# Performance work log

Hardware: AMD Instinct MI355X
Metric: run time of the kernel (lower is better)

Reference implementation:

```python
import jax, jax.numpy as jnp
import numpy as np


def _bilinear_gather(img, y, x):
    """Bilinear sample img [B,C,H,W] at float coords y,x [B,K,H,W] with zero padding.
    Returns [B,C,K,H,W]."""
    B, C, H, W = img.shape
    K = y.shape[1]
    y0 = jnp.floor(y)
    x0 = jnp.floor(x)
    wy = y - y0  # fractional weights [B,K,H,W]
    wx = x - x0
    y0i = y0.astype(jnp.int32)
    x0i = x0.astype(jnp.int32)
    flat = img.reshape(B, C, 1, H * W)

    def gather(yi, xi):
        valid = (yi >= 0) & (yi < H) & (xi >= 0) & (xi < W)  # [B,K,H,W]
        idx = jnp.clip(yi, 0, H - 1) * W + jnp.clip(xi, 0, W - 1)
        v = jnp.take_along_axis(flat, idx.reshape(B, 1, K, H * W), axis=-1)
        v = v.reshape(B, C, K, H, W)
        return v * valid[:, None].astype(img.dtype)

    v00 = gather(y0i, x0i)
    v01 = gather(y0i, x0i + 1)
    v10 = gather(y0i + 1, x0i)
    v11 = gather(y0i + 1, x0i + 1)
    wy_ = wy[:, None]  # [B,1,K,H,W]
    wx_ = wx[:, None]
    return (v00 * (1 - wy_) * (1 - wx_) + v01 * (1 - wy_) * wx_
            + v10 * wy_ * (1 - wx_) + v11 * wy_ * wx_)


def deform_conv2d(inp, offsets, ker):
    """torchvision.ops.deform_conv2d with stride=1, dilation=1, padding=k//2, groups=1."""
    B, C, H, W = inp.shape
    Co, Ci, k, _ = ker.shape
    pad = k // 2
    K = k * k
    off = offsets.reshape(B, K, 2, H, W)
    dy = off[:, :, 0]  # [B,K,H,W] (y offset first per torchvision convention)
    dx = off[:, :, 1]
    ii, jj = jnp.meshgrid(jnp.arange(k), jnp.arange(k), indexing='ij')
    ky = ii.reshape(K).astype(inp.dtype)  # kernel tap row index
    kx = jj.reshape(K).astype(inp.dtype)
    hgrid = jnp.arange(H, dtype=inp.dtype)
    wgrid = jnp.arange(W, dtype=inp.dtype)
    # sampling coords: p = out_pos - pad + tap + offset
    y = dy + (hgrid[None, None, :, None] - pad) + ky[None, :, None, None]
    x = dx + (wgrid[None, None, None, :] - pad) + kx[None, :, None, None]
    sampled = _bilinear_gather(inp, y, x)  # [B,C,K,H,W]
    return jnp.einsum('bckhw,ock->bohw', sampled, ker.reshape(Co, Ci, K))


def setup_inputs() -> dict:
    key = jax.random.key(0)
    k1, k2, k3, k4 = jax.random.split(key, 4)
    B, C, H, W, Co, k = 4, 16, 256, 256, 16, 3
    offsets = jax.random.normal(k1, (B, 2 * k * k, H, W), dtype=jnp.float32)
    inp = jax.random.normal(k2, (B, C, H, W), dtype=jnp.float32)
    ker = jax.random.normal(k3, (Co, C, k, k), dtype=jnp.float32) * 0.1
    target = jax.random.normal(k4, (B, Co, H, W), dtype=jnp.float32)
    return {"offsets": offsets, "input": inp, "ker": ker, "target": target}


def reference(offsets, input, ker, target):
    deformed = deform_conv2d(input, offsets, ker)
    # criterion = MSELoss (mean reduction)
    loss = jnp.mean((deformed - target) ** 2)
    return loss
```

## Files before the change

### kernel.cpp

```cpp
#include <hip/hip_runtime.h>

#define B_  4
#define C_  16
#define H_  256
#define W_  256
#define CO_ 16
#define KS_ 3
#define KK_ 9
#define HW_ (H_ * W_)
#define IMG_WORDS ((size_t)B_ * HW_ * 8)
#define KER_OFF   IMG_WORDS
#define NKB 5
#define NBLK 2048
#define PART_OFF (KER_OFF + (size_t)NKB * 256)

typedef __attribute__((ext_vector_type(8))) short bf16x8;
typedef __attribute__((ext_vector_type(4))) float f32x4;
union U4S8 { uint4 u; bf16x8 s; };

#define LOBF(u) __uint_as_float((u) << 16)
#define HIBF(u) __uint_as_float((u) & 0xffff0000u)

__device__ __forceinline__ unsigned rne_bf16(float v) {
    unsigned b = __float_as_uint(v);
    return (b + 0x7fffu + ((b >> 16) & 1u)) >> 16;
}

__global__ __launch_bounds__(256) void pack_nhwc_bf16(
    const float* __restrict__ inp, const float* __restrict__ ker,
    unsigned* __restrict__ wsu)
{
    const int t = threadIdx.x;
    const int e = blockIdx.x * 256 + t;
    const int b = e >> 16;
    const int hw = e & (HW_ - 1);
    const float* src = inp + (size_t)b * (C_ * HW_) + hw;
    float v[C_];
#pragma unroll
    for (int c = 0; c < C_; c++)
        v[c] = src[c * HW_];
    unsigned u[8];
#pragma unroll
    for (int j = 0; j < 8; j++)
        u[j] = rne_bf16(v[2 * j]) | (rne_bf16(v[2 * j + 1]) << 16);
    uint4* dst = ((uint4*)wsu) + (size_t)e * 2;
    dst[0] = make_uint4(u[0], u[1], u[2], u[3]);
    dst[1] = make_uint4(u[4], u[5], u[6], u[7]);

    if (blockIdx.x == 0) {
        for (int i = t; i < NKB * 256; i += 256) {
            const int wj  = i & 3;
            const int l   = (i >> 2) & 63;
            const int blk = i >> 8;
            const int o   = l & 15;
            unsigned lo = 0, hi = 0;
            {
                int j = 2 * wj, k = (l >> 4) * 8 + j;
                int tap = 2 * blk + (k >> 4), c = k & 15;
                if (tap <= 8) lo = rne_bf16(ker[(o * C_ + c) * KK_ + tap]);
                j = 2 * wj + 1; k = (l >> 4) * 8 + j;
                tap = 2 * blk + (k >> 4); c = k & 15;
                if (tap <= 8) hi = rne_bf16(ker[(o * C_ + c) * KK_ + tap]);
            }
            wsu[KER_OFF + i] = lo | (hi << 16);
        }
    }
}

__device__ __forceinline__ void tap_setup(
    int h, int w, int kk, float dy, float dx,
    int* idx, float* wt)
{
    const float y = dy + (float)(h - 1 + kk / KS_);
    const float x = dx + (float)(w - 1 + kk % KS_);
    const float y0f = floorf(y);
    const float x0f = floorf(x);
    const int   y0  = (int)y0f;
    const int   x0  = (int)x0f;
    const float wy  = y - y0f;
    const float wx  = x - x0f;

    float w00 = (1.f - wy) * (1.f - wx);
    float w01 = (1.f - wy) * wx;
    float w10 = wy * (1.f - wx);
    float w11 = wy * wx;

    const bool v0y = ((unsigned)y0       < (unsigned)H_);
    const bool v1y = ((unsigned)(y0 + 1) < (unsigned)H_);
    const bool v0x = ((unsigned)x0       < (unsigned)W_);
    const bool v1x = ((unsigned)(x0 + 1) < (unsigned)W_);

    wt[0] = (v0y & v0x) ? w00 : 0.f;
    wt[1] = (v0y & v1x) ? w01 : 0.f;
    wt[2] = (v1y & v0x) ? w10 : 0.f;
    wt[3] = (v1y & v1x) ? w11 : 0.f;

    const int y0c = min(max(y0,     0), H_ - 1);
    const int y1c = min(max(y0 + 1, 0), H_ - 1);
    const int x0c = min(max(x0,     0), W_ - 1);
    const int x1c = min(max(x0 + 1, 0), W_ - 1);

    idx[0] = y0c * W_ + x0c;
    idx[1] = y0c * W_ + x1c;
    idx[2] = y1c * W_ + x0c;
    idx[3] = y1c * W_ + x1c;
}

__device__ __forceinline__ unsigned blendpack(
    unsigned a, unsigned b, unsigned c, unsigned d,
    float w0, float w1, float w2, float w3)
{
    const float lo = w0 * LOBF(a) + w1 * LOBF(b) + w2 * LOBF(c) + w3 * LOBF(d);
    const float hi = w0 * HIBF(a) + w1 * HIBF(b) + w2 * HIBF(c) + w3 * HIBF(d);
    return __builtin_amdgcn_perm(__float_as_uint(hi), __float_as_uint(lo),
                                 0x07060302u);
}

__global__ __launch_bounds__(256) void deform_loss_mfma(
    const float* __restrict__ off, const unsigned* __restrict__ wsu,
    const float* __restrict__ tgt, float* __restrict__ partials)
{
    const int f = (blockIdx.x & 7) * 256 + (blockIdx.x >> 3);
    const int t = threadIdx.x;
    const int l = t & 63;
    const int q = l >> 4;
    const int m = l & 15;
    const int base = f * 128 + (t >> 6) * 32;
    const int b    = base >> 16;
    const int hwb  = base & (HW_ - 1);
    const int h    = hwb >> 8;
    const int w0   = (hwb & (W_ - 1)) + m;

    const float* offp = off + (size_t)b * (2 * KK_ * HW_) + (size_t)h * W_;
    const uint4* ib   = ((const uint4*)wsu) + (size_t)b * HW_ * 2;
    const uint4* kb   = (const uint4*)(wsu + KER_OFF);

    bf16x8 bfr[NKB];
#pragma unroll
    for (int kbk = 0; kbk < NKB; kbk++) {
        U4S8 cv; cv.u = kb[kbk * 64 + l];
        bfr[kbk] = cv.s;
    }

    float dyv[2][NKB], dxv[2][NKB];
#pragma unroll
    for (int g = 0; g < 2; g++)
#pragma unroll
        for (int kbk = 0; kbk < NKB; kbk++) {
            const int tap = min(2 * kbk + (q >> 1), KK_ - 1);
            dyv[g][kbk] = offp[(size_t)(2 * tap) * HW_ + w0 + 16 * g];
            dxv[g][kbk] = offp[(size_t)(2 * tap + 1) * HW_ + w0 + 16 * g];
        }
    const float* tbase = tgt + (size_t)b * (CO_ * HW_) + (size_t)m * HW_
                       + hwb + 4 * q;
    const float4 tv0 = *(const float4*)(tbase);
    const float4 tv1 = *(const float4*)(tbase + 16);

    f32x4 acc[2] = {{0.f, 0.f, 0.f, 0.f}, {0.f, 0.f, 0.f, 0.f}};
    uint4 cor[2][4];
    float wts[2][4];

    {
        int idx[4];
        tap_setup(h, w0, min(q >> 1, KK_ - 1), dyv[0][0], dxv[0][0], idx, wts[0]);
#pragma unroll
        for (int i = 0; i < 4; i++) cor[0][i] = ib[idx[i] * 2 + (q & 1)];
    }

#pragma unroll
    for (int kbi = 0; kbi < 2 * NKB; kbi++) {
        const int cur = kbi & 1, nxt = cur ^ 1;
        if (kbi + 1 < 2 * NKB) {
            const int gn = (kbi + 1) / NKB, kn = (kbi + 1) % NKB;
            int idx[4];
            tap_setup(h, w0 + 16 * gn, min(2 * kn + (q >> 1), KK_ - 1),
                      dyv[gn][kn], dxv[gn][kn], idx, wts[nxt]);
#pragma unroll
            for (int i = 0; i < 4; i++) cor[nxt][i] = ib[idx[i] * 2 + (q & 1)];
        }

        const int g = kbi / NKB, kkb = kbi % NKB;
        const float w0_ = wts[cur][0], w1_ = wts[cur][1],
                    w2_ = wts[cur][2], w3_ = wts[cur][3];
        const uint4 c0 = cor[cur][0], c1 = cor[cur][1],
                    c2 = cor[cur][2], c3 = cor[cur][3];
        uint4 A4;
        A4.x = blendpack(c0.x, c1.x, c2.x, c3.x, w0_, w1_, w2_, w3_);
        A4.y = blendpack(c0.y, c1.y, c2.y, c3.y, w0_, w1_, w2_, w3_);
        A4.z = blendpack(c0.z, c1.z, c2.z, c3.z, w0_, w1_, w2_, w3_);
        A4.w = blendpack(c0.w, c1.w, c2.w, c3.w, w0_, w1_, w2_, w3_);
        U4S8 ca; ca.u = A4;

        acc[g] = __builtin_amdgcn_mfma_f32_16x16x32_bf16(ca.s, bfr[kkb],
                                                         acc[g], 0, 0, 0);
    }

    float d0 = acc[0][0] - tv0.x, d1 = acc[0][1] - tv0.y,
          d2 = acc[0][2] - tv0.z, d3 = acc[0][3] - tv0.w;
    float e0 = acc[1][0] - tv1.x, e1 = acc[1][1] - tv1.y,
          e2 = acc[1][2] - tv1.z, e3 = acc[1][3] - tv1.w;
    float part = (d0 * d0 + d1 * d1 + d2 * d2 + d3 * d3
                + e0 * e0 + e1 * e1 + e2 * e2 + e3 * e3)
               * (1.0f / (float)((size_t)B_ * CO_ * HW_));

#pragma unroll
    for (int sft = 32; sft > 0; sft >>= 1)
        part += __shfl_down(part, sft, 64);

    __shared__ float red[4];
    if (l == 0)
        red[t >> 6] = part;
    __syncthreads();
    if (t == 0)
        partials[blockIdx.x] = red[0] + red[1] + red[2] + red[3];
}

__global__ __launch_bounds__(256) void reduce_partials(
    const float* __restrict__ partials, float* __restrict__ out)
{
    const int t = threadIdx.x;
    float s = 0.f;
#pragma unroll
    for (int i = 0; i < NBLK / 256; i++)
        s += partials[t + i * 256];
#pragma unroll
    for (int sft = 32; sft > 0; sft >>= 1)
        s += __shfl_down(s, sft, 64);
    __shared__ float red[4];
    if ((t & 63) == 0) red[t >> 6] = s;
    __syncthreads();
    if (t == 0) out[0] = red[0] + red[1] + red[2] + red[3];
}

__global__ __launch_bounds__(256) void deform_loss_kernel(
    const float* __restrict__ off, const float* __restrict__ inp,
    const float* __restrict__ ker, const float* __restrict__ tgt,
    float* __restrict__ out)
{
    const int idx = blockIdx.x * blockDim.x + threadIdx.x;
    float part = 0.f;
    if (idx < B_ * H_ * W_) {
        const int w  = idx & (W_ - 1);
        const int h  = (idx >> 8) & (H_ - 1);
        const int b  = idx >> 16;
        const int hw = h * W_ + w;
        const float* offb = off + (size_t)b * (2 * KK_ * HW_);
        const float* inpb = inp + (size_t)b * (C_ * HW_);
        float acc[CO_];
#pragma unroll
        for (int o = 0; o < CO_; o++) acc[o] = 0.f;
        for (int kk = 0; kk < KK_; kk++) {
            const float dy = offb[(2 * kk)     * HW_ + hw];
            const float dx = offb[(2 * kk + 1) * HW_ + hw];
            const float y = dy + (float)(h - 1 + kk / KS_);
            const float x = dx + (float)(w - 1 + kk % KS_);
            const float y0f = floorf(y);
            const float x0f = floorf(x);
            const int   y0  = (int)y0f;
            const int   x0  = (int)x0f;
            const float wy  = y - y0f;
            const float wx  = x - x0f;
            float w00 = (1.f - wy) * (1.f - wx);
            float w01 = (1.f - wy) * wx;
            float w10 = wy * (1.f - wx);
            float w11 = wy * wx;
            const bool v0y = ((unsigned)y0       < (unsigned)H_);
            const bool v1y = ((unsigned)(y0 + 1) < (unsigned)H_);
            const bool v0x = ((unsigned)x0       < (unsigned)W_);
            const bool v1x = ((unsigned)(x0 + 1) < (unsigned)W_);
            w00 = (v0y & v0x) ? w00 : 0.f;
            w01 = (v0y & v1x) ? w01 : 0.f;
            w10 = (v1y & v0x) ? w10 : 0.f;
            w11 = (v1y & v1x) ? w11 : 0.f;
            const int i00 = min(max(y0,0),H_-1)*W_ + min(max(x0,0),W_-1);
            const int i01 = min(max(y0,0),H_-1)*W_ + min(max(x0+1,0),W_-1);
            const int i10 = min(max(y0+1,0),H_-1)*W_ + min(max(x0,0),W_-1);
            const int i11 = min(max(y0+1,0),H_-1)*W_ + min(max(x0+1,0),W_-1);
            for (int c = 0; c < C_; c++) {
                const float* pp = inpb + c * HW_;
                const float s = pp[i00]*w00 + pp[i01]*w01 + pp[i10]*w10 + pp[i11]*w11;
#pragma unroll
                for (int o = 0; o < CO_; o++)
                    acc[o] = fmaf(s, ker[(o * C_ + c) * KK_ + kk], acc[o]);
            }
        }
        const float* tb = tgt + (size_t)b * (CO_ * HW_);
#pragma unroll
        for (int o = 0; o < CO_; o++) {
            const float d = acc[o] - tb[o * HW_ + hw];
            part = fmaf(d, d, part);
        }
        part *= (1.0f / (float)((size_t)B_ * CO_ * HW_));
    }
#pragma unroll
    for (int sft = 32; sft > 0; sft >>= 1)
        part += __shfl_down(part, sft, 64);
    if ((threadIdx.x & 63) == 0)
        atomicAdd(out, part);
}

extern "C" void kernel_launch(void* const* d_in, const int* in_sizes, int n_in,
                              void* d_out, int out_size, void* d_ws, size_t ws_size,
                              hipStream_t stream) {
    const float* offsets = (const float*)d_in[0];
    const float* input   = (const float*)d_in[1];
    const float* ker     = (const float*)d_in[2];
    const float* target  = (const float*)d_in[3];
    float* out = (float*)d_out;

    const size_t need = (PART_OFF + NBLK) * sizeof(unsigned);
    if (ws_size >= need) {
        unsigned* wsu = (unsigned*)d_ws;
        pack_nhwc_bf16<<<(B_ * HW_) / 256, 256, 0, stream>>>(input, ker, wsu);
        deform_loss_mfma<<<NBLK, 256, 0, stream>>>(
            offsets, wsu, target, (float*)(wsu + PART_OFF));
        reduce_partials<<<1, 256, 0, stream>>>(
            (const float*)(wsu + PART_OFF), out);
    } else {
        hipMemsetAsync(out, 0, sizeof(float), stream);
        const int total = B_ * H_ * W_;
        deform_loss_kernel<<<(total + 255) / 256, 256, 0, stream>>>(
            offsets, input, ker, target, out);
    }
}
```

Before: 114.3 us.

## Drop reduce kernel via atomics, vectorize blend, skip padded tap gathers

```diff
diff --git a/kernel.cpp b/kernel.cpp
--- a/kernel.cpp
+++ b/kernel.cpp
@@ -12,10 +12,10 @@
 #define KER_OFF   IMG_WORDS
 #define NKB 5
 #define NBLK 2048
-#define PART_OFF (KER_OFF + (size_t)NKB * 256)
 
 typedef __attribute__((ext_vector_type(8))) short bf16x8;
 typedef __attribute__((ext_vector_type(4))) float f32x4;
+typedef __attribute__((ext_vector_type(2))) float f32x2;
 union U4S8 { uint4 u; bf16x8 s; };
 
 #define LOBF(u) __uint_as_float((u) << 16)
@@ -28,7 +28,7 @@
 
 __global__ __launch_bounds__(256) void pack_nhwc_bf16(
     const float* __restrict__ inp, const float* __restrict__ ker,
-    unsigned* __restrict__ wsu)
+    unsigned* __restrict__ wsu, float* __restrict__ out)
 {
     const int t = threadIdx.x;
     const int e = blockIdx.x * 256 + t;
@@ -48,6 +48,7 @@
     dst[1] = make_uint4(u[4], u[5], u[6], u[7]);
 
     if (blockIdx.x == 0) {
+        if (t == 0) out[0] = 0.f;
         for (int i = t; i < NKB * 256; i += 256) {
             const int wj  = i & 3;
             const int l   = (i >> 2) & 63;
@@ -110,15 +111,21 @@
     unsigned a, unsigned b, unsigned c, unsigned d,
     float w0, float w1, float w2, float w3)
 {
-    const float lo = w0 * LOBF(a) + w1 * LOBF(b) + w2 * LOBF(c) + w3 * LOBF(d);
-    const float hi = w0 * HIBF(a) + w1 * HIBF(b) + w2 * HIBF(c) + w3 * HIBF(d);
-    return __builtin_amdgcn_perm(__float_as_uint(hi), __float_as_uint(lo),
+    f32x2 va = {LOBF(a), HIBF(a)};
+    f32x2 vb = {LOBF(b), HIBF(b)};
+    f32x2 vc = {LOBF(c), HIBF(c)};
+    f32x2 vd = {LOBF(d), HIBF(d)};
+    f32x2 r = va * w0;
+    r += vb * w1;
+    r += vc * w2;
+    r += vd * w3;
+    return __builtin_amdgcn_perm(__float_as_uint(r.y), __float_as_uint(r.x),
                                  0x07060302u);
 }
 
 __global__ __launch_bounds__(256) void deform_loss_mfma(
     const float* __restrict__ off, const unsigned* __restrict__ wsu,
-    const float* __restrict__ tgt, float* __restrict__ partials)
+    const float* __restrict__ tgt, float* __restrict__ out)
 {
     const int f = (blockIdx.x & 7) * 256 + (blockIdx.x >> 3);
     const int t = threadIdx.x;
@@ -162,7 +169,7 @@
 
     {
         int idx[4];
-        tap_setup(h, w0, min(q >> 1, KK_ - 1), dyv[0][0], dxv[0][0], idx, wts[0]);
+        tap_setup(h, w0, q >> 1, dyv[0][0], dxv[0][0], idx, wts[0]);
 #pragma unroll
         for (int i = 0; i < 4; i++) cor[0][i] = ib[idx[i] * 2 + (q & 1)];
     }
@@ -175,11 +182,20 @@
             int idx[4];
             tap_setup(h, w0 + 16 * gn, min(2 * kn + (q >> 1), KK_ - 1),
                       dyv[gn][kn], dxv[gn][kn], idx, wts[nxt]);
+            if (kn == NKB - 1) {
+                const bool pad = (q >> 1) != 0;
+                if (pad) {
+                    wts[nxt][0] = 0.f; wts[nxt][1] = 0.f;
+                    wts[nxt][2] = 0.f; wts[nxt][3] = 0.f;
+                    idx[0] = 0; idx[1] = 0; idx[2] = 0; idx[3] = 0;
+                }
+            }
 #pragma unroll
             for (int i = 0; i < 4; i++) cor[nxt][i] = ib[idx[i] * 2 + (q & 1)];
         }
 
-        const int g = kbi / NKB, kkb = kbi % NKB;
+        const int g = kbi / NKB;
+        const int kkb = kbi % NKB;
         const float w0_ = wts[cur][0], w1_ = wts[cur][1],
                     w2_ = wts[cur][2], w3_ = wts[cur][3];
         const uint4 c0 = cor[cur][0], c1 = cor[cur][1],
@@ -212,24 +228,7 @@
         red[t >> 6] = part;
     __syncthreads();
     if (t == 0)
-        partials[blockIdx.x] = red[0] + red[1] + red[2] + red[3];
-}
-
-__global__ __launch_bounds__(256) void reduce_partials(
-    const float* __restrict__ partials, float* __restrict__ out)
-{
-    const int t = threadIdx.x;
-    float s = 0.f;
-#pragma unroll
-    for (int i = 0; i < NBLK / 256; i++)
-        s += partials[t + i * 256];
-#pragma unroll
-    for (int sft = 32; sft > 0; sft >>= 1)
-        s += __shfl_down(s, sft, 64);
-    __shared__ float red[4];
-    if ((t & 63) == 0) red[t >> 6] = s;
-    __syncthreads();
-    if (t == 0) out[0] = red[0] + red[1] + red[2] + red[3];
+        atomicAdd(out, red[0] + red[1] + red[2] + red[3]);
 }
 
 __global__ __launch_bounds__(256) void deform_loss_kernel(
@@ -308,14 +307,12 @@
     const float* target  = (const float*)d_in[3];
     float* out = (float*)d_out;
 
-    const size_t need = (PART_OFF + NBLK) * sizeof(unsigned);
+    const size_t need = (KER_OFF + (size_t)NKB * 256) * sizeof(unsigned);
     if (ws_size >= need) {
         unsigned* wsu = (unsigned*)d_ws;
-        pack_nhwc_bf16<<<(B_ * HW_) / 256, 256, 0, stream>>>(input, ker, wsu);
-        deform_loss_mfma<<<NBLK, 256, 0, stream>>>(
-            offsets, wsu, target, (float*)(wsu + PART_OFF));
-        reduce_partials<<<1, 256, 0, stream>>>(
-            (const float*)(wsu + PART_OFF), out);
+        pack_nhwc_bf16<<<(B_ * HW_) / 256, 256, 0, stream>>>(
+            input, ker, wsu, out);
+        deform_loss_mfma<<<NBLK, 256, 0, stream>>>(offsets, wsu, target, out);
     } else {
         hipMemsetAsync(out, 0, sizeof(float), stream);
         const int total = B_ * H_ * W_;
```

After: 125.5 us. 9.7% more time.
